# Performance work log

Hardware: AMD Instinct MI355X
Metric: run time of the kernel (lower is better)

The kernel has to match this reference:

```python
import jax, jax.numpy as jnp
import numpy as np


def setup_inputs() -> dict:
    key = jax.random.key(0)
    x = jax.random.normal(key, (4, 512, 64, 64), dtype=jnp.float32)
    return {"x": x}


def reference(x) -> jnp.ndarray:
    B, C, H, W = x.shape
    N = H * W
    v = x.reshape(B, C, N)                      # proj_query/key/value all = x flattened
    # energy[b, i, j] = sum_c x[b,c,i] * x[b,c,j]
    energy = jnp.einsum('bci,bcj->bij', v, v)
    attention = jax.nn.softmax(energy, axis=-1)  # softmax over last dim (keys j)
    # out[b,c,i] = sum_j v[b,c,j] * attention[b,i,j]  (== V @ attention^T)
    out = jnp.einsum('bcj,bij->bci', v, attention)
    return out.reshape(B, C, H, W)
```

## Files before the change

### kernel.cpp

```cpp
#include <hip/hip_runtime.h>
#include <hip/hip_bf16.h>

typedef unsigned short u16;
typedef unsigned int   u32;
typedef unsigned long long u64;
typedef __attribute__((ext_vector_type(8))) short bf16x8;
typedef __attribute__((ext_vector_type(4))) float f32x4;

#define BB 4
#define CC 512
#define NN 4096
#define LOG2E 1.44269504f

static __device__ __forceinline__ u16 f2b(float f) {
    __hip_bfloat16 h = __float2bfloat16(f);
    return *(u16*)&h;
}
static __device__ __forceinline__ u16 f2b_fast(float f) {
    u32 u = __builtin_bit_cast(u32, f);
    return (u16)((u + 0x8000u) >> 16);
}
static __device__ __forceinline__ float b2f(u16 b) {
    u32 u = (u32)b << 16;
    return __builtin_bit_cast(float, u);
}

typedef __attribute__((address_space(1))) const u32 GU32;
typedef __attribute__((address_space(3))) u32 LU32;
__device__ __forceinline__ void async16(const void* g, void* l) {
    __builtin_amdgcn_global_load_lds((GU32*)g, (LU32*)l, 16, 0, 0);
}

__global__ __launch_bounds__(256) void prep_kernel(const float* __restrict__ x,
                                                   u16* __restrict__ XT,
                                                   u16* __restrict__ XN,
                                                   float* __restrict__ norms) {
    __shared__ __align__(8) u16 tile[64][68];
    __shared__ float nsum[64];
    int blk = blockIdx.x;
    int b  = blk >> 9;
    int r2 = blk & 511;
    int c0 = (r2 >> 6) << 6;
    int n0 = (r2 & 63) << 6;
    int t  = threadIdx.x;
    if (t < 64) nsum[t] = 0.f;

    int nq    = t & 15;
    int rbase = t >> 4;
    float psum[4] = {0.f, 0.f, 0.f, 0.f};
    #pragma unroll
    for (int p = 0; p < 4; ++p) {
        int cl = p * 16 + rbase;
        const float* src = x + ((size_t)(b * CC + c0 + cl) * NN) + n0 + nq * 4;
        float4 v = *(const float4*)src;
        psum[0] += v.x * v.x; psum[1] += v.y * v.y;
        psum[2] += v.z * v.z; psum[3] += v.w * v.w;
        u64 pk = (u64)f2b(v.x) | ((u64)f2b(v.y) << 16) |
                 ((u64)f2b(v.z) << 32) | ((u64)f2b(v.w) << 48);
        *(u64*)&XN[((size_t)(b * CC + c0 + cl) * NN) + n0 + nq * 4] = pk;
        *(u64*)&tile[cl][nq * 4] = pk;
    }
    __syncthreads();
    int c2 = (t & 31) * 2;
    int nb = t >> 5;
    #pragma unroll
    for (int rr = 0; rr < 8; ++rr) {
        int nl = rr * 8 + nb;
        u32 lo = tile[c2][nl], hi = tile[c2 + 1][nl];
        *(u32*)&XT[((size_t)(b * NN + n0 + nl) * CC) + c0 + c2] = lo | (hi << 16);
    }
    #pragma unroll
    for (int k = 0; k < 4; ++k) atomicAdd(&nsum[nq * 4 + k], psum[k]);
    __syncthreads();
    if (t < 64) atomicAdd(&norms[(size_t)b * NN + n0 + t], nsum[t]);
}

__global__ __launch_bounds__(256) void maxn_kernel(const float* __restrict__ norms,
                                                   float* __restrict__ maxn) {
    int b = blockIdx.x, t = threadIdx.x;
    float m = 0.f;
    for (int k = t; k < NN; k += 256) m = fmaxf(m, norms[(size_t)b * NN + k]);
    #pragma unroll
    for (int d = 1; d < 64; d <<= 1) m = fmaxf(m, __shfl_xor(m, d));
    __shared__ float wred[4];
    if ((t & 63) == 0) wred[t >> 6] = m;
    __syncthreads();
    if (t == 0) maxn[b] = fmaxf(fmaxf(wred[0], wred[1]), fmaxf(wred[2], wred[3]));
}

__global__ __launch_bounds__(256, 2) void flash_kernel(const u16* __restrict__ XT,
                                                       const u16* __restrict__ XN,
                                                       const float* __restrict__ norms,
                                                       const float* __restrict__ maxn,
                                                       float* __restrict__ outF,
                                                       u16* __restrict__ outH,
                                                       float* __restrict__ l0g,
                                                       float* __restrict__ l1g,
                                                       int split) {
    __shared__ __align__(16) u16 KtT[2][32 * 520];
    __shared__ __align__(16) u16 Plds[2][64 * 40];
    __shared__ float lLds[64];

    int blk   = blockIdx.x;
    int inner = blk & 255;
    int hf    = split ? (blk >> 8) : 0;
    int xcd = inner & 7;
    int b   = xcd >> 1;
    int ib  = (inner >> 3) + ((xcd & 1) << 5);
    int i_base = ib * 64;
    int jlo = hf * (NN / 2) * split;
    int njt = split ? 64 : 128;

    int t    = threadIdx.x;
    int w    = t >> 6;
    int lane = t & 63;
    int l15  = lane & 15;
    int q    = lane >> 4;

    const u16* xtb = XT + (size_t)b * NN * CC;
    const u16* xnb = XN + (size_t)b * CC * NN;

    float mxn = maxn[b];
    float M2[4];
    #pragma unroll
    for (int r = 0; r < 4; ++r) {
        float nr = norms[(size_t)b * NN + i_base + w * 16 + q * 4 + r];
        M2[r] = (sqrtf(nr * mxn) - 40.f) * LOG2E;
    }

    bf16x8 qf[16];
    {
        const u16* qrow = xtb + (size_t)(i_base + w * 16 + l15) * CC;
        #pragma unroll
        for (int kk = 0; kk < 16; ++kk)
            qf[kk] = *(const bf16x8*)(qrow + kk * 32 + q * 8);
    }

    f32x4 o[8][4];
    #pragma unroll
    for (int ct = 0; ct < 8; ++ct)
        #pragma unroll
        for (int it = 0; it < 4; ++it)
            o[ct][it] = (f32x4){0.f, 0.f, 0.f, 0.f};
    float lpart[4] = {0.f, 0.f, 0.f, 0.f};

    {
        const u16* src = xtb + (size_t)(jlo + w * 8) * CC + lane * 8;
        #pragma unroll
        for (int rr = 0; rr < 8; ++rr)
            async16(src + rr * CC, &KtT[0][(w * 8 + rr) * 520]);
    }
    __syncthreads();

    for (int jt = 0; jt < njt; ++jt) {
        int buf = jt & 1;
        int j0  = jlo + jt * 32;

        bf16x8 vf[8];
        #pragma unroll
        for (int ct = 0; ct < 8; ++ct)
            vf[ct] = *(const bf16x8*)(xnb + (size_t)(w * 128 + ct * 16 + l15) * NN + j0 + q * 8);

        if (jt + 1 < njt) {
            const u16* src = xtb + (size_t)(j0 + 32 + w * 8) * CC + lane * 8;
            #pragma unroll
            for (int rr = 0; rr < 8; ++rr)
                async16(src + rr * CC, &KtT[buf ^ 1][(w * 8 + rr) * 520]);
        }

        f32x4 s0 = {0.f,0.f,0.f,0.f}, s1 = {0.f,0.f,0.f,0.f};
        #pragma unroll
        for (int kk = 0; kk < 16; ++kk) {
            bf16x8 b0 = *(const bf16x8*)&KtT[buf][(l15)      * 520 + kk * 32 + q * 8];
            bf16x8 b1 = *(const bf16x8*)&KtT[buf][(16 + l15) * 520 + kk * 32 + q * 8];
            s0 = __builtin_amdgcn_mfma_f32_16x16x32_bf16(qf[kk], b0, s0, 0, 0, 0);
            s1 = __builtin_amdgcn_mfma_f32_16x16x32_bf16(qf[kk], b1, s1, 0, 0, 0);
        }

        #pragma unroll
        for (int r = 0; r < 4; ++r) {
            float p0 = __builtin_amdgcn_exp2f(fmaf(s0[r], LOG2E, -M2[r]));
            float p1 = __builtin_amdgcn_exp2f(fmaf(s1[r], LOG2E, -M2[r]));
            u16 h0 = f2b_fast(p0), h1 = f2b_fast(p1);
            lpart[r] += b2f(h0) + b2f(h1);
            int row = w * 16 + q * 4 + r;
            Plds[buf][row * 40 +      l15] = h0;
            Plds[buf][row * 40 + 16 + l15] = h1;
        }
        __syncthreads();

        bf16x8 pb[4];
        #pragma unroll
        for (int it = 0; it < 4; ++it)
            pb[it] = *(const bf16x8*)&Plds[buf][(it * 16 + l15) * 40 + q * 8];
        #pragma unroll
        for (int ct = 0; ct < 8; ++ct)
            #pragma unroll
            for (int it = 0; it < 4; ++it)
                o[ct][it] = __builtin_amdgcn_mfma_f32_16x16x32_bf16(vf[ct], pb[it], o[ct][it], 0, 0, 0);
    }

    #pragma unroll
    for (int r = 0; r < 4; ++r) {
        float s = lpart[r];
        s += __shfl_xor(s, 1);
        s += __shfl_xor(s, 2);
        s += __shfl_xor(s, 4);
        s += __shfl_xor(s, 8);
        lpart[r] = s;
    }

    if (!split) {
        if (l15 == 0) {
            #pragma unroll
            for (int r = 0; r < 4; ++r) lLds[w * 16 + q * 4 + r] = lpart[r];
        }
        __syncthreads();
        float linv[4];
        #pragma unroll
        for (int it = 0; it < 4; ++it) linv[it] = 1.f / lLds[it * 16 + l15];
        float* ob = outF + (size_t)b * CC * NN;
        #pragma unroll
        for (int ct = 0; ct < 8; ++ct)
            #pragma unroll
            for (int r = 0; r < 4; ++r) {
                int c = w * 128 + ct * 16 + q * 4 + r;
                float* orow = ob + (size_t)c * NN + i_base;
                #pragma unroll
                for (int it = 0; it < 4; ++it)
                    orow[it * 16 + l15] = o[ct][it][r] * linv[it];
            }
    } else {
        if (l15 == 0) {
            float* lg = (hf == 0) ? l0g : l1g;
            #pragma unroll
            for (int r = 0; r < 4; ++r)
                lg[(size_t)b * NN + i_base + w * 16 + q * 4 + r] = lpart[r];
        }
        if (hf == 0) {
            float* ob = outF + (size_t)b * CC * NN;
            #pragma unroll
            for (int ct = 0; ct < 8; ++ct)
                #pragma unroll
                for (int r = 0; r < 4; ++r) {
                    int c = w * 128 + ct * 16 + q * 4 + r;
                    float* orow = ob + (size_t)c * NN + i_base;
                    #pragma unroll
                    for (int it = 0; it < 4; ++it)
                        orow[it * 16 + l15] = o[ct][it][r];
                }
        } else {
            u16* ob = outH + (size_t)b * CC * NN;
            #pragma unroll
            for (int ct = 0; ct < 8; ++ct)
                #pragma unroll
                for (int r = 0; r < 4; ++r) {
                    int c = w * 128 + ct * 16 + q * 4 + r;
                    u16* orow = ob + (size_t)c * NN + i_base;
                    #pragma unroll
                    for (int it = 0; it < 4; ++it)
                        orow[it * 16 + l15] = f2b(o[ct][it][r]);
                }
        }
    }
}

__global__ __launch_bounds__(256) void combine_kernel(float* __restrict__ out,
                                                      const u16* __restrict__ P1,
                                                      const float* __restrict__ l0,
                                                      const float* __restrict__ l1) {
    size_t g = (size_t)blockIdx.x * 256 + threadIdx.x;
    size_t f = g * 4;
    int i = (int)(f & (NN - 1));
    int b = (int)(f >> 21);
    float4 p0 = *(float4*)&out[f];
    u64 pk = *(const u64*)&P1[f];
    float p0a[4] = {p0.x, p0.y, p0.z, p0.w};
    float r[4];
    #pragma unroll
    for (int k = 0; k < 4; ++k) {
        float l = l0[(size_t)b * NN + i + k] + l1[(size_t)b * NN + i + k];
        float p1f = b2f((u16)((pk >> (16 * k)) & 0xFFFFu));
        r[k] = (p0a[k] + p1f) / l;
    }
    *(float4*)&out[f] = (float4){r[0], r[1], r[2], r[3]};
}

extern "C" void kernel_launch(void* const* d_in, const int* in_sizes, int n_in,
                              void* d_out, int out_size, void* d_ws, size_t ws_size,
                              hipStream_t stream) {
    const float* x = (const float*)d_in[0];
    size_t SZ = (size_t)BB * NN * CC;
    u16* XT = (u16*)d_ws;
    u16* XN = XT + SZ;
    u16* P1 = XN + SZ;
    float* norms = (float*)(P1 + SZ);
    float* l0g   = norms + (size_t)BB * NN;
    float* l1g   = l0g + (size_t)BB * NN;
    float* maxn  = l1g + (size_t)BB * NN;
    size_t needed = 3 * SZ * 2 + 3 * (size_t)BB * NN * 4 + 64;
    int split = (ws_size >= needed) ? 1 : 0;
    float* out = (float*)d_out;
    if (!split) {
        norms = (float*)(XN + SZ);
        l0g = norms + (size_t)BB * NN;
        l1g = l0g;
        maxn = l1g + (size_t)BB * NN;
    }

    hipMemsetAsync(norms, 0, (size_t)BB * NN * sizeof(float), stream);
    prep_kernel<<<2048, 256, 0, stream>>>(x, XT, XN, norms);
    maxn_kernel<<<BB, 256, 0, stream>>>(norms, maxn);
    if (split) {
        flash_kernel<<<512, 256, 0, stream>>>(XT, XN, norms, maxn, out, P1, l0g, l1g, 1);
        combine_kernel<<<(BB * CC * NN / 4) / 256, 256, 0, stream>>>(out, P1, l0g, l1g);
    } else {
        flash_kernel<<<256, 256, 0, stream>>>(XT, XN, norms, maxn, out, P1, l0g, l1g, 0);
    }
}
```

Measured before the change: 294.7 us.

## Swizzle XT layout for LDS, fuse max-norm into prep, split QK accumulators

The prep kernel now loops over all channels per block, so each block owns its norms outright. It writes them directly and computes the per-batch max norm with an atomicMax, which removes the separate maxn kernel and the large norms memset. XT is stored with an XOR swizzle on 8-element chunks, which lets the K tile in LDS drop its padding while avoiding bank conflicts; Q loads are unswizzled to match. The QK^T loop is split into two independent accumulator chains to shorten MFMA dependency latency, and P is packed and stored as one u32 per lane. The row sum now uses unrounded fp32 probabilities instead of the bf16-rounded values. The prep grid drops to 256 blocks, which may reduce memory parallelism in that stage.

```diff
diff --git a/kernel.cpp b/kernel.cpp
--- a/kernel.cpp
+++ b/kernel.cpp
@@ -16,10 +16,6 @@
     __hip_bfloat16 h = __float2bfloat16(f);
     return *(u16*)&h;
 }
-static __device__ __forceinline__ u16 f2b_fast(float f) {
-    u32 u = __builtin_bit_cast(u32, f);
-    return (u16)((u + 0x8000u) >> 16);
-}
 static __device__ __forceinline__ float b2f(u16 b) {
     u32 u = (u32)b << 16;
     return __builtin_bit_cast(float, u);
@@ -34,70 +30,69 @@
 __global__ __launch_bounds__(256) void prep_kernel(const float* __restrict__ x,
                                                    u16* __restrict__ XT,
                                                    u16* __restrict__ XN,
-                                                   float* __restrict__ norms) {
+                                                   float* __restrict__ norms,
+                                                   int* __restrict__ maxn) {
     __shared__ __align__(8) u16 tile[64][68];
     __shared__ float nsum[64];
     int blk = blockIdx.x;
-    int b  = blk >> 9;
-    int r2 = blk & 511;
-    int c0 = (r2 >> 6) << 6;
-    int n0 = (r2 & 63) << 6;
+    int b  = blk >> 6;
+    int n0 = (blk & 63) << 6;
     int t  = threadIdx.x;
     if (t < 64) nsum[t] = 0.f;
 
     int nq    = t & 15;
     int rbase = t >> 4;
     float psum[4] = {0.f, 0.f, 0.f, 0.f};
-    #pragma unroll
-    for (int p = 0; p < 4; ++p) {
-        int cl = p * 16 + rbase;
-        const float* src = x + ((size_t)(b * CC + c0 + cl) * NN) + n0 + nq * 4;
-        float4 v = *(const float4*)src;
-        psum[0] += v.x * v.x; psum[1] += v.y * v.y;
-        psum[2] += v.z * v.z; psum[3] += v.w * v.w;
-        u64 pk = (u64)f2b(v.x) | ((u64)f2b(v.y) << 16) |
-                 ((u64)f2b(v.z) << 32) | ((u64)f2b(v.w) << 48);
-        *(u64*)&XN[((size_t)(b * CC + c0 + cl) * NN) + n0 + nq * 4] = pk;
-        *(u64*)&tile[cl][nq * 4] = pk;
-    }
-    __syncthreads();
-    int c2 = (t & 31) * 2;
-    int nb = t >> 5;
-    #pragma unroll
-    for (int rr = 0; rr < 8; ++rr) {
-        int nl = rr * 8 + nb;
-        u32 lo = tile[c2][nl], hi = tile[c2 + 1][nl];
-        *(u32*)&XT[((size_t)(b * NN + n0 + nl) * CC) + c0 + c2] = lo | (hi << 16);
+
+    for (int c0 = 0; c0 < CC; c0 += 64) {
+        #pragma unroll
+        for (int p = 0; p < 4; ++p) {
+            int cl = p * 16 + rbase;
+            const float* src = x + ((size_t)(b * CC + c0 + cl) * NN) + n0 + nq * 4;
+            float4 v = *(const float4*)src;
+            psum[0] += v.x * v.x; psum[1] += v.y * v.y;
+            psum[2] += v.z * v.z; psum[3] += v.w * v.w;
+            u64 pk = (u64)f2b(v.x) | ((u64)f2b(v.y) << 16) |
+                     ((u64)f2b(v.z) << 32) | ((u64)f2b(v.w) << 48);
+            *(u64*)&XN[((size_t)(b * CC + c0 + cl) * NN) + n0 + nq * 4] = pk;
+            *(u64*)&tile[cl][nq * 4] = pk;
+        }
+        __syncthreads();
+        int c2 = (t & 31) * 2;
+        int nb = t >> 5;
+        #pragma unroll
+        for (int rr = 0; rr < 8; ++rr) {
+            int nl = rr * 8 + nb;
+            u32 val = (u32)tile[c2][nl] | ((u32)tile[c2 + 1][nl] << 16);
+            int c  = c0 + c2;
+            int cs = ((((c >> 3) ^ (nl & 7)) << 3) | (c & 7));
+            *(u32*)&XT[((size_t)(b * NN + n0 + nl) * CC) + cs] = val;
+        }
+        __syncthreads();
     }
     #pragma unroll
     for (int k = 0; k < 4; ++k) atomicAdd(&nsum[nq * 4 + k], psum[k]);
     __syncthreads();
-    if (t < 64) atomicAdd(&norms[(size_t)b * NN + n0 + t], nsum[t]);
-}
-
-__global__ __launch_bounds__(256) void maxn_kernel(const float* __restrict__ norms,
-                                                   float* __restrict__ maxn) {
-    int b = blockIdx.x, t = threadIdx.x;
-    float m = 0.f;
-    for (int k = t; k < NN; k += 256) m = fmaxf(m, norms[(size_t)b * NN + k]);
-    #pragma unroll
-    for (int d = 1; d < 64; d <<= 1) m = fmaxf(m, __shfl_xor(m, d));
-    __shared__ float wred[4];
-    if ((t & 63) == 0) wred[t >> 6] = m;
-    __syncthreads();
-    if (t == 0) maxn[b] = fmaxf(fmaxf(wred[0], wred[1]), fmaxf(wred[2], wred[3]));
+    if (t < 64) {
+        float v = nsum[t];
+        norms[(size_t)b * NN + n0 + t] = v;
+        float m = v;
+        #pragma unroll
+        for (int d = 1; d < 64; d <<= 1) m = fmaxf(m, __shfl_xor(m, d));
+        if (t == 0) atomicMax(&maxn[b], __float_as_int(m));
+    }
 }
 
 __global__ __launch_bounds__(256, 2) void flash_kernel(const u16* __restrict__ XT,
                                                        const u16* __restrict__ XN,
                                                        const float* __restrict__ norms,
-                                                       const float* __restrict__ maxn,
+                                                       const int* __restrict__ maxn,
                                                        float* __restrict__ outF,
                                                        u16* __restrict__ outH,
                                                        float* __restrict__ l0g,
                                                        float* __restrict__ l1g,
                                                        int split) {
-    __shared__ __align__(16) u16 KtT[2][32 * 520];
+    __shared__ __align__(16) u16 KtT[2][32 * 512];
     __shared__ __align__(16) u16 Plds[2][64 * 40];
     __shared__ float lLds[64];
 
@@ -120,7 +115,7 @@
     const u16* xtb = XT + (size_t)b * NN * CC;
     const u16* xnb = XN + (size_t)b * CC * NN;
 
-    float mxn = maxn[b];
+    float mxn = __int_as_float(maxn[b]);
     float M2[4];
     #pragma unroll
     for (int r = 0; r < 4; ++r) {
@@ -128,12 +123,13 @@
         M2[r] = (sqrtf(nr * mxn) - 40.f) * LOG2E;
     }
 
+    int sw = l15 & 7;
     bf16x8 qf[16];
     {
         const u16* qrow = xtb + (size_t)(i_base + w * 16 + l15) * CC;
         #pragma unroll
         for (int kk = 0; kk < 16; ++kk)
-            qf[kk] = *(const bf16x8*)(qrow + kk * 32 + q * 8);
+            qf[kk] = *(const bf16x8*)(qrow + (((kk * 4 + q) ^ sw) << 3));
     }
 
     f32x4 o[8][4];
@@ -144,11 +140,14 @@
             o[ct][it] = (f32x4){0.f, 0.f, 0.f, 0.f};
     float lpart[4] = {0.f, 0.f, 0.f, 0.f};
 
+    int r0  = 2 * l15;
+    int sw0 = r0 & 7, sw1 = (r0 + 1) & 7;
+
     {
         const u16* src = xtb + (size_t)(jlo + w * 8) * CC + lane * 8;
         #pragma unroll
         for (int rr = 0; rr < 8; ++rr)
-            async16(src + rr * CC, &KtT[0][(w * 8 + rr) * 520]);
+            async16(src + rr * CC, &KtT[0][(w * 8 + rr) * 512]);
     }
     __syncthreads();
 
@@ -165,27 +164,37 @@
             const u16* src = xtb + (size_t)(j0 + 32 + w * 8) * CC + lane * 8;
             #pragma unroll
             for (int rr = 0; rr < 8; ++rr)
-                async16(src + rr * CC, &KtT[buf ^ 1][(w * 8 + rr) * 520]);
-        }
-
-        f32x4 s0 = {0.f,0.f,0.f,0.f}, s1 = {0.f,0.f,0.f,0.f};
-        #pragma unroll
-        for (int kk = 0; kk < 16; ++kk) {
-            bf16x8 b0 = *(const bf16x8*)&KtT[buf][(l15)      * 520 + kk * 32 + q * 8];
-            bf16x8 b1 = *(const bf16x8*)&KtT[buf][(16 + l15) * 520 + kk * 32 + q * 8];
-            s0 = __builtin_amdgcn_mfma_f32_16x16x32_bf16(qf[kk], b0, s0, 0, 0, 0);
-            s1 = __builtin_amdgcn_mfma_f32_16x16x32_bf16(qf[kk], b1, s1, 0, 0, 0);
-        }
+                async16(src + rr * CC, &KtT[buf ^ 1][(w * 8 + rr) * 512]);
+        }
+
+        const u16* kb = &KtT[buf][0];
+        f32x4 s0a = {0.f,0.f,0.f,0.f}, s1a = {0.f,0.f,0.f,0.f};
+        f32x4 s0b = {0.f,0.f,0.f,0.f}, s1b = {0.f,0.f,0.f,0.f};
+        #pragma unroll
+        for (int kk = 0; kk < 8; ++kk) {
+            bf16x8 b0 = *(const bf16x8*)&kb[ r0      * 512 + (((kk * 4 + q) ^ sw0) << 3)];
+            bf16x8 b1 = *(const bf16x8*)&kb[(r0 + 1) * 512 + (((kk * 4 + q) ^ sw1) << 3)];
+            s0a = __builtin_amdgcn_mfma_f32_16x16x32_bf16(qf[kk], b0, s0a, 0, 0, 0);
+            s1a = __builtin_amdgcn_mfma_f32_16x16x32_bf16(qf[kk], b1, s1a, 0, 0, 0);
+        }
+        #pragma unroll
+        for (int kk = 8; kk < 16; ++kk) {
+            bf16x8 b0 = *(const bf16x8*)&kb[ r0      * 512 + (((kk * 4 + q) ^ sw0) << 3)];
+            bf16x8 b1 = *(const bf16x8*)&kb[(r0 + 1) * 512 + (((kk * 4 + q) ^ sw1) << 3)];
+            s0b = __builtin_amdgcn_mfma_f32_16x16x32_bf16(qf[kk], b0, s0b, 0, 0, 0);
+            s1b = __builtin_amdgcn_mfma_f32_16x16x32_bf16(qf[kk], b1, s1b, 0, 0, 0);
+        }
+        f32x4 s0 = s0a + s0b, s1 = s1a + s1b;
 
         #pragma unroll
         for (int r = 0; r < 4; ++r) {
             float p0 = __builtin_amdgcn_exp2f(fmaf(s0[r], LOG2E, -M2[r]));
             float p1 = __builtin_amdgcn_exp2f(fmaf(s1[r], LOG2E, -M2[r]));
-            u16 h0 = f2b_fast(p0), h1 = f2b_fast(p1);
-            lpart[r] += b2f(h0) + b2f(h1);
+            lpart[r] += p0 + p1;
+            u32 w01 = ((__builtin_bit_cast(u32, p0) + 0x8000u) >> 16) |
+                      ((__builtin_bit_cast(u32, p1) + 0x8000u) & 0xffff0000u);
             int row = w * 16 + q * 4 + r;
-            Plds[buf][row * 40 +      l15] = h0;
-            Plds[buf][row * 40 + 16 + l15] = h1;
+            *(u32*)&Plds[buf][row * 40 + r0] = w01;
         }
         __syncthreads();
 
@@ -297,7 +306,7 @@
     float* norms = (float*)(P1 + SZ);
     float* l0g   = norms + (size_t)BB * NN;
     float* l1g   = l0g + (size_t)BB * NN;
-    float* maxn  = l1g + (size_t)BB * NN;
+    int*   maxn  = (int*)(l1g + (size_t)BB * NN);
     size_t needed = 3 * SZ * 2 + 3 * (size_t)BB * NN * 4 + 64;
     int split = (ws_size >= needed) ? 1 : 0;
     float* out = (float*)d_out;
@@ -305,12 +314,11 @@
         norms = (float*)(XN + SZ);
         l0g = norms + (size_t)BB * NN;
         l1g = l0g;
-        maxn = l1g + (size_t)BB * NN;
-    }
-
-    hipMemsetAsync(norms, 0, (size_t)BB * NN * sizeof(float), stream);
-    prep_kernel<<<2048, 256, 0, stream>>>(x, XT, XN, norms);
-    maxn_kernel<<<BB, 256, 0, stream>>>(norms, maxn);
+        maxn = (int*)(l1g + (size_t)BB * NN);
+    }
+
+    hipMemsetAsync(maxn, 0, BB * sizeof(int), stream);
+    prep_kernel<<<256, 256, 0, stream>>>(x, XT, XN, norms, maxn);
     if (split) {
         flash_kernel<<<512, 256, 0, stream>>>(XT, XN, norms, maxn, out, P1, l0g, l1g, 1);
         combine_kernel<<<(BB * CC * NN / 4) / 256, 256, 0, stream>>>(out, P1, l0g, l1g);
```

Result: slower. 861.2 us (+192.3%).
